# Performance work log

Measured on AMD Instinct MI355X. Metric: run time of the kernel, lower is better.

## Reference

```python
import jax, jax.numpy as jnp
import numpy as np

N_NODES = 500_000
N_EDGES = 8_000_000
D_FEAT = 64


def setup_inputs() -> dict:
    key = jax.random.key(0)
    k_x, k_v, k_r, k_c = jax.random.split(key, 4)
    x = jax.random.normal(k_x, (N_NODES, D_FEAT), dtype=jnp.float32)
    edge_vals = jax.random.uniform(k_v, (N_EDGES,), dtype=jnp.float32)
    row = jax.random.randint(k_r, (N_EDGES,), 0, N_NODES, dtype=jnp.int32)
    col = jax.random.randint(k_c, (N_EDGES,), 0, N_NODES, dtype=jnp.int32)
    return {"x": x, "edge_vals": edge_vals, "row": row, "col": col}


def reference(x, edge_vals, row, col):
    # out = A @ x where A is sparse with A[row[e], col[e]] = edge_vals[e]
    # gather source features, scale by edge value, segment-sum into rows
    msgs = edge_vals[:, None] * x[col]          # [E, d]
    out = jax.ops.segment_sum(msgs, row, num_segments=N_NODES)  # [N, d]
    return out
```

## Files before the change

### kernel.cpp

```cpp
#include <hip/hip_runtime.h>


#define D_FEAT 64
#define RPB 256
#define BKT_SHIFT 8
#define MAX_BKT 2048
#define TILE_EDGES 8192
#define EPT 32
#define TILE_BIN 32768
#define BIN_THREADS 1024
#define CAP 6144

typedef float vf4 __attribute__((ext_vector_type(4)));

__global__ __launch_bounds__(256)
void hist_kernel(const int* __restrict__ row, int* __restrict__ cnt_g,
                 int n_edges, int kb) {
    __shared__ int cnt[MAX_BKT];
    for (int i = threadIdx.x; i < kb; i += 256) cnt[i] = 0;
    __syncthreads();
    int base = blockIdx.x * TILE_EDGES;
#pragma unroll
    for (int k = 0; k < EPT; k++) {
        int e = base + k * 256 + threadIdx.x;
        if (e < n_edges) atomicAdd(&cnt[row[e] >> BKT_SHIFT], 1);
    }
    __syncthreads();
    for (int i = threadIdx.x; i < kb; i += 256) {
        int c = cnt[i];
        if (c) atomicAdd(&cnt_g[i], c);
    }
}

__global__ __launch_bounds__(256)
void scan_kernel(const int* __restrict__ cnt_g, int* __restrict__ start,
                 int* __restrict__ gcursor, int kb) {
    __shared__ int sums[256];
    int vals[8];
    int base = threadIdx.x * 8;
    int s = 0;
#pragma unroll
    for (int i = 0; i < 8; i++) {
        int idx = base + i;
        int v = (idx < kb) ? cnt_g[idx] : 0;
        s += v;
        vals[i] = s;
    }
    sums[threadIdx.x] = s;
    __syncthreads();
    for (int off = 1; off < 256; off <<= 1) {
        int t = (threadIdx.x >= off) ? sums[threadIdx.x - off] : 0;
        __syncthreads();
        sums[threadIdx.x] += t;
        __syncthreads();
    }
    int toff = (threadIdx.x > 0) ? sums[threadIdx.x - 1] : 0;
#pragma unroll
    for (int i = 0; i < 8; i++) {
        int idx = base + i;
        if (idx < kb) {
            int incl = vals[i] + toff;
            int v = vals[i] - (i ? vals[i - 1] : 0);
            start[idx + 1] = incl;
            gcursor[idx] = incl - v;
        }
    }
    if (threadIdx.x == 0) start[0] = 0;
}

__global__ __launch_bounds__(BIN_THREADS)
void bin_kernel(const int* __restrict__ row, const int* __restrict__ col,
                const float* __restrict__ val,
                int* __restrict__ gcursor, int2* __restrict__ packed,
                int n_edges, int kb) {
    __shared__ int cnt[MAX_BKT];
    __shared__ int base_s[MAX_BKT];
    for (int i = threadIdx.x; i < kb; i += BIN_THREADS) cnt[i] = 0;
    __syncthreads();
    int tbase = blockIdx.x * TILE_BIN;
    int r_[EPT];
#pragma unroll
    for (int k = 0; k < EPT; k++) {
        int e = tbase + k * BIN_THREADS + threadIdx.x;
        int r = (e < n_edges) ? row[e] : -1;
        r_[k] = r;
        if (r >= 0) atomicAdd(&cnt[r >> BKT_SHIFT], 1);
    }
    __syncthreads();
    for (int i = threadIdx.x; i < kb; i += BIN_THREADS) {
        int c = cnt[i];
        base_s[i] = c ? atomicAdd(&gcursor[i], c) : 0;
        cnt[i] = 0;
    }
    __syncthreads();
#pragma unroll
    for (int k = 0; k < EPT; k++) {
        int r = r_[k];
        if (r >= 0) {
            int e = tbase + k * BIN_THREADS + threadIdx.x;
            int b = r >> BKT_SHIFT;
            int rank = atomicAdd(&cnt[b], 1);
            packed[base_s[b] + rank] =
                make_int2(((r & (RPB - 1)) << 19) | col[e], __float_as_int(val[e]));
        }
    }
}

__global__ __launch_bounds__(1024)
void sort_reduce(const float* __restrict__ x, const int2* __restrict__ packed,
                 const int* __restrict__ start, float* __restrict__ out,
                 int n_nodes) {
    __shared__ int2 ed[CAP];
    __shared__ unsigned short inv[CAP];
    __shared__ int cnt[RPB];
    __shared__ int sc[RPB];
    __shared__ int cur[RPB];

    const int tid = threadIdx.x;
    const int b = blockIdx.x;
    const int s = start[b];
    const int e = start[b + 1];
    const int n = e - s;

    const int g = tid >> 4;
    const int l16 = tid & 15;
    const vf4* x4 = (const vf4*)x;
    vf4* out4 = (vf4*)out;
    const long long rbase = (long long)b * RPB;

    if (n <= CAP) {
        if (tid < RPB) cnt[tid] = 0;
        __syncthreads();

        const long long* pk = (const long long*)packed;
        for (int i = tid; i < n; i += 1024) {
            long long pv = __builtin_nontemporal_load(&pk[s + i]);
            int2 r;
            r.x = (int)pv;
            r.y = (int)(pv >> 32);
            ed[i] = r;
            atomicAdd(&cnt[((unsigned)r.x) >> 19], 1);
        }
        __syncthreads();

        if (tid < RPB) sc[tid] = cnt[tid];
        __syncthreads();
        for (int off = 1; off < RPB; off <<= 1) {
            int t = 0;
            if (tid < RPB && tid >= off) t = sc[tid - off];
            __syncthreads();
            if (tid < RPB) sc[tid] += t;
            __syncthreads();
        }
        if (tid < RPB) cur[tid] = (tid > 0) ? sc[tid - 1] : 0;
        __syncthreads();

        for (int i = tid; i < n; i += 1024) {
            int lr = ((unsigned)ed[i].x) >> 19;
            int d = atomicAdd(&cur[lr], 1);
            inv[d] = (unsigned short)i;
        }
        __syncthreads();

#pragma unroll
        for (int p = 0; p < 4; p++) {
            int r = p * 64 + g;
            int rs = r ? sc[r - 1] : 0;
            int re = sc[r];
            vf4 a = (vf4)0.f;
            int j = rs;
            for (; j + 3 < re; j += 4) {
                int i0 = inv[j], i1 = inv[j + 1], i2 = inv[j + 2], i3 = inv[j + 3];
                int2 e0 = ed[i0], e1 = ed[i1], e2 = ed[i2], e3 = ed[i3];
                vf4 x0 = x4[(size_t)(e0.x & 0x7FFFF) * 16 + l16];
                vf4 x1 = x4[(size_t)(e1.x & 0x7FFFF) * 16 + l16];
                vf4 x2 = x4[(size_t)(e2.x & 0x7FFFF) * 16 + l16];
                vf4 x3 = x4[(size_t)(e3.x & 0x7FFFF) * 16 + l16];
                a += __int_as_float(e0.y) * x0;
                a += __int_as_float(e1.y) * x1;
                a += __int_as_float(e2.y) * x2;
                a += __int_as_float(e3.y) * x3;
            }
            for (; j < re; j++) {
                int i0 = inv[j];
                int2 e0 = ed[i0];
                vf4 x0 = x4[(size_t)(e0.x & 0x7FFFF) * 16 + l16];
                a += __int_as_float(e0.y) * x0;
            }
            long long rg = rbase + r;
            if (rg < n_nodes)
                __builtin_nontemporal_store(a, &out4[rg * 16 + l16]);
        }
    } else {
#pragma unroll
        for (int p = 0; p < 4; p++) {
            int r = p * 64 + g;
            vf4 a = (vf4)0.f;
            for (int i = s; i < e; i++) {
                int2 e0 = packed[i];
                if ((int)(((unsigned)e0.x) >> 19) == r) {
                    vf4 x0 = x4[(size_t)(e0.x & 0x7FFFF) * 16 + l16];
                    a += __int_as_float(e0.y) * x0;
                }
            }
            long long rg = rbase + r;
            if (rg < n_nodes)
                __builtin_nontemporal_store(a, &out4[rg * 16 + l16]);
        }
    }
}

__global__ __launch_bounds__(256)
void graphconv_scatter(const float* __restrict__ x, const float* __restrict__ edge_vals,
                       const int* __restrict__ row, const int* __restrict__ col,
                       float* __restrict__ out, int n_edges) {
    int tid = blockIdx.x * blockDim.x + threadIdx.x;
    int lane16 = tid & 15;
    int e = tid >> 4;
    if (e >= n_edges) return;
    int r = row[e];
    int c = col[e];
    float v = edge_vals[e];
    const float4* xs = (const float4*)(x + (size_t)c * D_FEAT);
    float4 xv = xs[lane16];
    float* o = out + (size_t)r * D_FEAT + lane16 * 4;
    atomicAdd(o + 0, v * xv.x);
    atomicAdd(o + 1, v * xv.y);
    atomicAdd(o + 2, v * xv.z);
    atomicAdd(o + 3, v * xv.w);
}

extern "C" void kernel_launch(void* const* d_in, const int* in_sizes, int n_in,
                              void* d_out, int out_size, void* d_ws, size_t ws_size,
                              hipStream_t stream) {
    const float* x         = (const float*)d_in[0];
    const float* edge_vals = (const float*)d_in[1];
    const int*   row       = (const int*)d_in[2];
    const int*   col       = (const int*)d_in[3];
    float* out = (float*)d_out;

    const int n_nodes = in_sizes[0] / D_FEAT;
    const int n_edges = in_sizes[1];
    const int kb = (n_nodes + RPB - 1) >> BKT_SHIFT;

    size_t off = 0;
    auto alloc = [&](size_t bytes) {
        size_t p = off;
        off += (bytes + 255) & ~size_t(255);
        return p;
    };
    size_t o_start    = alloc((size_t)(kb + 1) * sizeof(int));
    size_t o_gcursor  = alloc((size_t)kb * sizeof(int));
    size_t o_cnt      = alloc((size_t)kb * sizeof(int));
    size_t o_packed   = alloc((size_t)n_edges * sizeof(int2));

    if (kb > MAX_BKT || n_nodes > (1 << 19) || off > ws_size) {
        hipMemsetAsync(d_out, 0, (size_t)out_size * sizeof(float), stream);
        long long total_threads = (long long)n_edges * 16;
        int grid = (int)((total_threads + 255) / 256);
        graphconv_scatter<<<grid, 256, 0, stream>>>(x, edge_vals, row, col, out, n_edges);
        return;
    }

    char* wsb = (char*)d_ws;
    int*  start     = (int*)(wsb + o_start);
    int*  gcursor   = (int*)(wsb + o_gcursor);
    int*  cnt_g     = (int*)(wsb + o_cnt);
    int2* packed    = (int2*)(wsb + o_packed);

    const int nblksH = (n_edges + TILE_EDGES - 1) / TILE_EDGES;
    const int nblksB = (n_edges + TILE_BIN - 1) / TILE_BIN;

    hipMemsetAsync(cnt_g, 0, (size_t)kb * sizeof(int), stream);
    hist_kernel<<<nblksH, 256, 0, stream>>>(row, cnt_g, n_edges, kb);
    scan_kernel<<<1, 256, 0, stream>>>(cnt_g, start, gcursor, kb);
    bin_kernel<<<nblksB, BIN_THREADS, 0, stream>>>(row, col, edge_vals, gcursor,
                                                   packed, n_edges, kb);
    sort_reduce<<<kb, 1024, 0, stream>>>(x, packed, start, out, n_nodes);
}
```

Baseline: 722.4 us.

## Coarsen buckets to 1024 rows and split each across four sub-blocks

Bucketing now uses 1024-row buckets, so there are 4x fewer global buckets and less contention and fragmentation in the binning scatter. Each bucket is handled by four reduce blocks, and each block filters the bucket's edges down to its 256-row quarter using ballot-based compaction into shared memory. The hist and bin kernels now share a 32K-edge tile with 1024 threads. The bin kernel rereads row from global memory instead of keeping it in registers. The trade-off is that each bucket's packed edges are read four times by the reduce blocks.

```diff
diff --git a/kernel.cpp b/kernel.cpp
--- a/kernel.cpp
+++ b/kernel.cpp
@@ -2,31 +2,31 @@
 
 
 #define D_FEAT 64
+#define RPM 1024
 #define RPB 256
-#define BKT_SHIFT 8
-#define MAX_BKT 2048
-#define TILE_EDGES 8192
+#define BKT_SHIFT 10
+#define MAX_BKT 512
+#define TILE 32768
 #define EPT 32
-#define TILE_BIN 32768
-#define BIN_THREADS 1024
+#define NTHR 1024
 #define CAP 6144
 
 typedef float vf4 __attribute__((ext_vector_type(4)));
 
-__global__ __launch_bounds__(256)
+__global__ __launch_bounds__(NTHR)
 void hist_kernel(const int* __restrict__ row, int* __restrict__ cnt_g,
                  int n_edges, int kb) {
     __shared__ int cnt[MAX_BKT];
-    for (int i = threadIdx.x; i < kb; i += 256) cnt[i] = 0;
-    __syncthreads();
-    int base = blockIdx.x * TILE_EDGES;
+    for (int i = threadIdx.x; i < kb; i += NTHR) cnt[i] = 0;
+    __syncthreads();
+    int base = blockIdx.x * TILE;
 #pragma unroll
     for (int k = 0; k < EPT; k++) {
-        int e = base + k * 256 + threadIdx.x;
+        int e = base + k * NTHR + threadIdx.x;
         if (e < n_edges) atomicAdd(&cnt[row[e] >> BKT_SHIFT], 1);
     }
     __syncthreads();
-    for (int i = threadIdx.x; i < kb; i += 256) {
+    for (int i = threadIdx.x; i < kb; i += NTHR) {
         int c = cnt[i];
         if (c) atomicAdd(&cnt_g[i], c);
     }
@@ -68,26 +68,23 @@
     if (threadIdx.x == 0) start[0] = 0;
 }
 
-__global__ __launch_bounds__(BIN_THREADS)
+__global__ __launch_bounds__(NTHR)
 void bin_kernel(const int* __restrict__ row, const int* __restrict__ col,
                 const float* __restrict__ val,
                 int* __restrict__ gcursor, int2* __restrict__ packed,
                 int n_edges, int kb) {
     __shared__ int cnt[MAX_BKT];
     __shared__ int base_s[MAX_BKT];
-    for (int i = threadIdx.x; i < kb; i += BIN_THREADS) cnt[i] = 0;
-    __syncthreads();
-    int tbase = blockIdx.x * TILE_BIN;
-    int r_[EPT];
+    for (int i = threadIdx.x; i < kb; i += NTHR) cnt[i] = 0;
+    __syncthreads();
+    int tbase = blockIdx.x * TILE;
 #pragma unroll
     for (int k = 0; k < EPT; k++) {
-        int e = tbase + k * BIN_THREADS + threadIdx.x;
-        int r = (e < n_edges) ? row[e] : -1;
-        r_[k] = r;
-        if (r >= 0) atomicAdd(&cnt[r >> BKT_SHIFT], 1);
-    }
-    __syncthreads();
-    for (int i = threadIdx.x; i < kb; i += BIN_THREADS) {
+        int e = tbase + k * NTHR + threadIdx.x;
+        if (e < n_edges) atomicAdd(&cnt[row[e] >> BKT_SHIFT], 1);
+    }
+    __syncthreads();
+    for (int i = threadIdx.x; i < kb; i += NTHR) {
         int c = cnt[i];
         base_s[i] = c ? atomicAdd(&gcursor[i], c) : 0;
         cnt[i] = 0;
@@ -95,18 +92,18 @@
     __syncthreads();
 #pragma unroll
     for (int k = 0; k < EPT; k++) {
-        int r = r_[k];
-        if (r >= 0) {
-            int e = tbase + k * BIN_THREADS + threadIdx.x;
+        int e = tbase + k * NTHR + threadIdx.x;
+        if (e < n_edges) {
+            int r = row[e];
             int b = r >> BKT_SHIFT;
             int rank = atomicAdd(&cnt[b], 1);
             packed[base_s[b] + rank] =
-                make_int2(((r & (RPB - 1)) << 19) | col[e], __float_as_int(val[e]));
-        }
-    }
-}
-
-__global__ __launch_bounds__(1024)
+                make_int2(((r & (RPM - 1)) << 19) | col[e], __float_as_int(val[e]));
+        }
+    }
+}
+
+__global__ __launch_bounds__(NTHR)
 void sort_reduce(const float* __restrict__ x, const int2* __restrict__ packed,
                  const int* __restrict__ start, float* __restrict__ out,
                  int n_nodes) {
@@ -115,34 +112,53 @@
     __shared__ int cnt[RPB];
     __shared__ int sc[RPB];
     __shared__ int cur[RPB];
+    __shared__ int ns_sh;
 
     const int tid = threadIdx.x;
-    const int b = blockIdx.x;
-    const int s = start[b];
-    const int e = start[b + 1];
-    const int n = e - s;
+    const int bm = blockIdx.x >> 2;
+    const int sb = blockIdx.x & 3;
+    const int s = start[bm];
+    const int e = start[bm + 1];
+    const int lane = tid & 63;
 
     const int g = tid >> 4;
     const int l16 = tid & 15;
     const vf4* x4 = (const vf4*)x;
     vf4* out4 = (vf4*)out;
-    const long long rbase = (long long)b * RPB;
-
-    if (n <= CAP) {
-        if (tid < RPB) cnt[tid] = 0;
-        __syncthreads();
-
-        const long long* pk = (const long long*)packed;
-        for (int i = tid; i < n; i += 1024) {
-            long long pv = __builtin_nontemporal_load(&pk[s + i]);
-            int2 r;
-            r.x = (int)pv;
-            r.y = (int)(pv >> 32);
-            ed[i] = r;
-            atomicAdd(&cnt[((unsigned)r.x) >> 19], 1);
-        }
-        __syncthreads();
-
+    const long long rbase = (long long)bm * RPM + (long long)sb * RPB;
+
+    if (tid == 0) ns_sh = 0;
+    if (tid < RPB) cnt[tid] = 0;
+    __syncthreads();
+
+    const long long* pk = (const long long*)packed;
+    for (int ib = s; ib < e; ib += NTHR) {
+        int i = ib + tid;
+        bool m = false;
+        int px = 0, py = 0;
+        if (i < e) {
+            long long pv = __builtin_nontemporal_load(&pk[i]);
+            px = (int)pv;
+            py = (int)(pv >> 32);
+            m = (((px >> 27) & 3) == sb);
+        }
+        unsigned long long mk = __ballot(m);
+        if (mk) {
+            int leader = __builtin_ctzll(mk);
+            int base = 0;
+            if (lane == leader) base = atomicAdd(&ns_sh, __popcll(mk));
+            base = __shfl(base, leader);
+            if (m) {
+                int d = base + __popcll(mk & ((1ull << lane) - 1));
+                if (d < CAP) ed[d] = make_int2(px, py);
+                atomicAdd(&cnt[(px >> 19) & 255], 1);
+            }
+        }
+    }
+    __syncthreads();
+    const int nf = ns_sh;
+
+    if (nf <= CAP) {
         if (tid < RPB) sc[tid] = cnt[tid];
         __syncthreads();
         for (int off = 1; off < RPB; off <<= 1) {
@@ -155,8 +171,8 @@
         if (tid < RPB) cur[tid] = (tid > 0) ? sc[tid - 1] : 0;
         __syncthreads();
 
-        for (int i = tid; i < n; i += 1024) {
-            int lr = ((unsigned)ed[i].x) >> 19;
+        for (int i = tid; i < nf; i += NTHR) {
+            int lr = (ed[i].x >> 19) & 255;
             int d = atomicAdd(&cur[lr], 1);
             inv[d] = (unsigned short)i;
         }
@@ -195,10 +211,11 @@
 #pragma unroll
         for (int p = 0; p < 4; p++) {
             int r = p * 64 + g;
+            int lt = (sb << 8) | r;
             vf4 a = (vf4)0.f;
             for (int i = s; i < e; i++) {
                 int2 e0 = packed[i];
-                if ((int)(((unsigned)e0.x) >> 19) == r) {
+                if (((e0.x >> 19) & 1023) == lt) {
                     vf4 x0 = x4[(size_t)(e0.x & 0x7FFFF) * 16 + l16];
                     a += __int_as_float(e0.y) * x0;
                 }
@@ -241,7 +258,7 @@
 
     const int n_nodes = in_sizes[0] / D_FEAT;
     const int n_edges = in_sizes[1];
-    const int kb = (n_nodes + RPB - 1) >> BKT_SHIFT;
+    const int kb = (n_nodes + RPM - 1) >> BKT_SHIFT;
 
     size_t off = 0;
     auto alloc = [&](size_t bytes) {
@@ -268,13 +285,12 @@
     int*  cnt_g     = (int*)(wsb + o_cnt);
     int2* packed    = (int2*)(wsb + o_packed);
 
-    const int nblksH = (n_edges + TILE_EDGES - 1) / TILE_EDGES;
-    const int nblksB = (n_edges + TILE_BIN - 1) / TILE_BIN;
+    const int nblks = (n_edges + TILE - 1) / TILE;
 
     hipMemsetAsync(cnt_g, 0, (size_t)kb * sizeof(int), stream);
-    hist_kernel<<<nblksH, 256, 0, stream>>>(row, cnt_g, n_edges, kb);
+    hist_kernel<<<nblks, NTHR, 0, stream>>>(row, cnt_g, n_edges, kb);
     scan_kernel<<<1, 256, 0, stream>>>(cnt_g, start, gcursor, kb);
-    bin_kernel<<<nblksB, BIN_THREADS, 0, stream>>>(row, col, edge_vals, gcursor,
-                                                   packed, n_edges, kb);
-    sort_reduce<<<kb, 1024, 0, stream>>>(x, packed, start, out, n_nodes);
-}
+    bin_kernel<<<nblks, NTHR, 0, stream>>>(row, col, edge_vals, gcursor,
+                                           packed, n_edges, kb);
+    sort_reduce<<<kb * 4, NTHR, 0, stream>>>(x, packed, start, out, n_nodes);
+}
```

New measurement: 657.5 us. 1.1x faster.
